# Optimization experiments

Measured on AMD Instinct MI355X. Metric: run time of the kernel, lower is better.

## Reference

```python
import jax, jax.numpy as jnp
import numpy as np

N = 50000   # nodes
E = 600000  # edges per relation
H = 4       # heads
DH = 32     # head dim (out_feat // num_heads)
D = 128     # in_feat == out_feat
NEG_SLOPE = 0.2


def setup_inputs() -> dict:
    key = jax.random.key(0)
    ks = jax.random.split(key, 13)
    x = jax.random.normal(ks[0], (N, D), jnp.float32)
    src_r0 = jax.random.randint(ks[1], (E,), 0, N, jnp.int32)
    dst_r0 = jax.random.randint(ks[2], (E,), 0, N, jnp.int32)
    src_r1 = jax.random.randint(ks[3], (E,), 0, N, jnp.int32)
    dst_r1 = jax.random.randint(ks[4], (E,), 0, N, jnp.int32)
    s = 0.05  # keep activations moderate (xavier-like scale)
    W_r0 = jax.random.normal(ks[5], (D, H * DH), jnp.float32) * s
    attn_l_r0 = jax.random.normal(ks[6], (H, DH), jnp.float32) * s
    attn_r_r0 = jax.random.normal(ks[7], (H, DH), jnp.float32) * s
    W_r1 = jax.random.normal(ks[8], (D, H * DH), jnp.float32) * s
    attn_l_r1 = jax.random.normal(ks[9], (H, DH), jnp.float32) * s
    attn_r_r1 = jax.random.normal(ks[10], (H, DH), jnp.float32) * s
    loop_weight = jax.random.normal(ks[11], (D, D), jnp.float32) * s
    h_bias = jnp.zeros((D,), jnp.float32)
    return {"x": x, "src_r0": src_r0, "dst_r0": dst_r0, "src_r1": src_r1,
            "dst_r1": dst_r1, "W_r0": W_r0, "attn_l_r0": attn_l_r0,
            "attn_r_r0": attn_r_r0, "W_r1": W_r1, "attn_l_r1": attn_l_r1,
            "attn_r_r1": attn_r_r1, "loop_weight": loop_weight, "h_bias": h_bias}


def _gat_rel(x, src, dst, W, attn_l, attn_r):
    """DGL GATConv for one relation: fc -> per-node attn scalars -> edge
    leaky_relu -> per-dst softmax -> weighted scatter-sum. Heads flattened."""
    feat = (x @ W).reshape(-1, H, DH)                 # [N, H, DH]
    el = jnp.einsum('nhd,hd->nh', feat, attn_l)       # [N, H]
    er = jnp.einsum('nhd,hd->nh', feat, attn_r)       # [N, H]
    e = jax.nn.leaky_relu(el[src] + er[dst], NEG_SLOPE)  # [E, H]
    # edge softmax per destination node, per head (numerically stable)
    m = jax.ops.segment_max(e, dst, num_segments=N)   # [N, H]
    ex = jnp.exp(e - m[dst])                          # [E, H]
    z = jax.ops.segment_sum(ex, dst, num_segments=N)  # [N, H]
    a = ex / z[dst]                                   # [E, H]
    msg = a[:, :, None] * feat[src]                   # [E, H, DH]
    out = jax.ops.segment_sum(msg, dst, num_segments=N)  # [N, H, DH]
    return out.reshape(-1, H * DH)                    # [N, D] (concat heads)


def reference(x, src_r0, dst_r0, src_r1, dst_r1, W_r0, attn_l_r0, attn_r_r0,
              W_r1, attn_l_r1, attn_r_r1, loop_weight, h_bias):
    # HeteroGraphConv with default 'sum' aggregation across relations
    h = _gat_rel(x, src_r0, dst_r0, W_r0, attn_l_r0, attn_r_r0)
    h = h + _gat_rel(x, src_r1, dst_r1, W_r1, attn_l_r1, attn_r_r1)
    # self-loop linear + bias + activation (dropout p=0.0 is identity)
    h = h + x @ loop_weight + h_bias
    return jax.nn.relu(h)
```

## Files before the change

### kernel.cpp

```cpp
#include <hip/hip_runtime.h>
#include <math.h>


#define CAP 48
#define NB 256
#define BCAP 2752
#define BIN_EDGES 2048

typedef __attribute__((ext_vector_type(8))) short short8v;
typedef __attribute__((ext_vector_type(4))) float float4v;

__device__ __forceinline__ unsigned short f2bf(float f) {
  unsigned int u = __float_as_uint(f);
  unsigned int r = (u + 0x7fffu + ((u >> 16) & 1u)) >> 16;
  return (unsigned short)r;
}
__device__ __forceinline__ float2 bfpair(unsigned int u) {
  float2 r;
  r.x = __uint_as_float(u << 16);
  r.y = __uint_as_float(u & 0xffff0000u);
  return r;
}

__global__ __launch_bounds__(256) void prep_bin_kernel(
    const float* __restrict__ W0, const float* __restrict__ W1,
    const float* __restrict__ WL,
    const float* __restrict__ al0, const float* __restrict__ ar0,
    const float* __restrict__ al1, const float* __restrict__ ar1,
    const int* __restrict__ src0, const int* __restrict__ dst0,
    const int* __restrict__ src1, const int* __restrict__ dst1,
    unsigned short* __restrict__ Wtall,
    unsigned int* __restrict__ bpair, int* __restrict__ gcnt,
    int E, int width, int nconvb, int nbin)
{
  __shared__ int smem[512];
  const int t = threadIdx.x;

  if ((int)blockIdx.x < nconvb) {
    const int j = blockIdx.x * 256 + t;
    if (j < 4096) {
      const int rel = j >> 11;
      const int q = j & 2047;
      const int n = q >> 4;
      const int k0 = (q & 15) * 8;
      const float* W = rel ? W1 : W0;
      unsigned short o[8];
#pragma unroll
      for (int u = 0; u < 8; ++u) o[u] = f2bf(W[(size_t)(k0 + u) * 128 + n]);
      *(short8v*)&Wtall[(size_t)rel * 18432 + n * 128 + k0] = *(short8v*)o;
    } else if (j < 4352) {
      const int e = j - 4096;
      const int rel = e >> 7;
      const int q = e & 127;
      const int cIdx = q >> 4;
      const int isr = cIdx >> 2;
      const int h = cIdx & 3;
      const int k0 = (q & 15) * 8;
      const float* W = rel ? W1 : W0;
      const float* av = isr ? (rel ? ar1 : ar0) : (rel ? al1 : al0);
      unsigned short o[8];
#pragma unroll
      for (int u = 0; u < 8; ++u) {
        float s = 0.f;
#pragma unroll
        for (int d = 0; d < 32; ++d)
          s += W[(size_t)(k0 + u) * 128 + h * 32 + d] * av[h * 32 + d];
        o[u] = f2bf(s);
      }
      *(short8v*)&Wtall[(size_t)rel * 18432 + (128 + cIdx) * 128 + k0] = *(short8v*)o;
    } else if (j < 4608) {
      const int e = j - 4352;
      const int rel = e >> 7;
      const int q = e & 127;
      const int cIdx = 136 + (q >> 4);
      const int k0 = (q & 15) * 8;
      const short8v z = {0,0,0,0,0,0,0,0};
      *(short8v*)&Wtall[(size_t)rel * 18432 + cIdx * 128 + k0] = z;
    } else if (j < 6656) {
      const int e = j - 4608;
      const int n = e >> 4;
      const int k0 = (e & 15) * 8;
      unsigned short o[8];
#pragma unroll
      for (int u = 0; u < 8; ++u) o[u] = f2bf(WL[(size_t)(k0 + u) * 128 + n]);
      *(short8v*)&Wtall[(size_t)2 * 18432 + n * 128 + k0] = *(short8v*)o;
    }
  } else {
    int* cnt = smem;
    int* gb  = smem + NB;
    const int bid = blockIdx.x - nconvb;
    const int rel = (bid >= nbin) ? 1 : 0;
    const int ib  = rel ? (bid - nbin) : bid;
    const int* srcA = rel ? src1 : src0;
    const int* dstA = rel ? dst1 : dst0;
    const int base = ib * BIN_EDGES;
    const int cntE = min(E - base, BIN_EDGES);

    for (int i = t; i < NB; i += 256) cnt[i] = 0;
    __syncthreads();

    unsigned int epack[8]; int eb[8], epos[8];
#pragma unroll
    for (int q = 0; q < 8; ++q) {
      const int ei = t * 8 + q;
      if (ei < cntE) {
        const int s = srcA[base + ei];
        const int d = dstA[base + ei];
        const int b = d / width;
        const int ld = d - b * width;
        epack[q] = (unsigned int)s | ((unsigned int)ld << 16);
        eb[q] = b;
        epos[q] = atomicAdd(&cnt[b], 1);
      } else {
        eb[q] = -1;
      }
    }
    __syncthreads();
    for (int i = t; i < NB; i += 256)
      gb[i] = atomicAdd(&gcnt[rel * NB + i], cnt[i]);
    __syncthreads();
#pragma unroll
    for (int q = 0; q < 8; ++q) {
      if (eb[q] >= 0) {
        const int slot = gb[eb[q]] + epos[q];
        if (slot < BCAP)
          bpair[(size_t)(rel * NB + eb[q]) * BCAP + slot] = epack[q];
      }
    }
  }
}

__global__ __launch_bounds__(256) void gemm_ell_kernel(
    const float* __restrict__ x, const unsigned short* __restrict__ Wtall,
    unsigned short* __restrict__ f0, unsigned short* __restrict__ f1,
    unsigned short* __restrict__ xl,
    float* __restrict__ el0, float* __restrict__ er0,
    float* __restrict__ el1, float* __restrict__ er1,
    const unsigned int* __restrict__ bpair, const int* __restrict__ gcnt,
    int* __restrict__ deg, int* __restrict__ ell0, int* __restrict__ ell1,
    int N, int width, int ngemm)
{
  __shared__ int ldeg[256];

  if ((int)blockIdx.x < ngemm) {
    const int wave = threadIdx.x >> 6, lane = threadIdx.x & 63;
    const int lr = lane & 15, lk = lane >> 4;
    const int row0 = blockIdx.x * 64 + wave * 16;
    const int r = row0 + lr;

    short8v a[4];
#pragma unroll
    for (int kc = 0; kc < 4; ++kc) {
      if (r < N) {
        const float* xp = &x[(size_t)r * 128 + kc * 32 + lk * 8];
        float4 u = *(const float4*)xp;
        float4 v = *(const float4*)(xp + 4);
        unsigned short o[8];
        o[0]=f2bf(u.x); o[1]=f2bf(u.y); o[2]=f2bf(u.z); o[3]=f2bf(u.w);
        o[4]=f2bf(v.x); o[5]=f2bf(v.y); o[6]=f2bf(v.z); o[7]=f2bf(v.w);
        a[kc] = *(short8v*)o;
      } else {
        a[kc] = (short8v){0,0,0,0,0,0,0,0};
      }
    }

#pragma unroll
    for (int w = 0; w < 3; ++w) {
      const unsigned short* Wp = Wtall + (size_t)w * 18432;
      const int NF = (w < 2) ? 9 : 8;
      float4v acc[9];
#pragma unroll
      for (int nf = 0; nf < 9; ++nf) acc[nf] = (float4v){0.f, 0.f, 0.f, 0.f};
      for (int nf = 0; nf < NF; ++nf) {
        const unsigned short* Bp = &Wp[(size_t)(nf * 16 + lr) * 128];
#pragma unroll
        for (int kc = 0; kc < 4; ++kc) {
          const short8v b = *(const short8v*)&Bp[kc * 32 + lk * 8];
          acc[nf] = __builtin_amdgcn_mfma_f32_16x16x32_bf16(a[kc], b, acc[nf], 0, 0, 0);
        }
      }

      unsigned short* dstp = (w == 0) ? f0 : (w == 1) ? f1 : xl;
#pragma unroll
      for (int nf = 0; nf < 8; ++nf) {
        const int col = nf * 16 + lr;
#pragma unroll
        for (int j = 0; j < 4; ++j) {
          const int row = row0 + lk * 4 + j;
          if (row < N) dstp[(size_t)row * 128 + col] = f2bf(acc[nf][j]);
        }
      }
      if (w < 2 && lr < 8) {
        float* ep = (lr < 4) ? (w ? el1 : el0) : (w ? er1 : er0);
        const int h = lr & 3;
#pragma unroll
        for (int j = 0; j < 4; ++j) {
          const int row = row0 + lk * 4 + j;
          if (row < N) ep[row * 4 + h] = acc[8][j];
        }
      }
    }
  } else {
    const int bid = blockIdx.x - ngemm;
    const int rel = bid >> 8;
    const int b = bid & 255;
    const int t = threadIdx.x;
    const int d0 = b * width;
    if (t < width) ldeg[t] = 0;
    __syncthreads();
    const int count = min(gcnt[rel * NB + b], BCAP);
    int* ell = rel ? ell1 : ell0;
    const unsigned int* bp = &bpair[(size_t)(rel * NB + b) * BCAP];
    for (int i = t; i < count; i += 256) {
      const unsigned int v = bp[i];
      const int src = (int)(v & 0xFFFFu);
      const int ld = (int)(v >> 16);
      const int slot = atomicAdd(&ldeg[ld], 1);
      if (slot < CAP) ell[(size_t)(d0 + ld) * CAP + slot] = src;
    }
    __syncthreads();
    if (t < width && d0 + t < N) deg[rel * N + d0 + t] = ldeg[t];
  }
}

__global__ __launch_bounds__(256) void gat_aggregate_kernel(
    const unsigned short* __restrict__ f0, const unsigned short* __restrict__ f1,
    const unsigned short* __restrict__ xl,
    const float* __restrict__ el0, const float* __restrict__ er0,
    const float* __restrict__ el1, const float* __restrict__ er1,
    const int* __restrict__ deg,
    const int* __restrict__ ell0, const int* __restrict__ ell1,
    const float* __restrict__ bias, float* __restrict__ out, int N)
{
  const int wid  = threadIdx.x >> 6;
  const int lane = threadIdx.x & 63;
  const int n = blockIdx.x * 4 + wid;
  if (n >= N) return;
  const int h  = lane >> 4;
  const int il = lane & 15;
  const int c  = lane * 2;
  const int pbase = lane & 48;

  float ox = 0.f, oy = 0.f;

#pragma unroll
  for (int rel = 0; rel < 2; ++rel) {
    const unsigned short* fb = rel ? f1 : f0;
    const float* el = rel ? el1 : el0;
    const float erh = (rel ? er1 : er0)[n * 4 + h];
    const int* ell = rel ? ell1 : ell0;
    const int d = min(deg[rel * N + n], CAP);

    float m = -INFINITY, sum = 0.f;
    float axa = 0.f, aya = 0.f, axb = 0.f, ayb = 0.f;
    for (int base = 0; base < d; base += 16) {
      const bool valid = (base + il) < d;
      int srcv = ell[(size_t)n * CAP + base + il];
      srcv = valid ? srcv : 0;
      float ev;
      {
        const float elv = el[srcv * 4 + h];
        float e2 = elv + erh;
        e2 = e2 > 0.f ? e2 : 0.2f * e2;
        ev = valid ? e2 : -INFINITY;
      }
      float cm = ev;
      cm = fmaxf(cm, __shfl_xor(cm, 1));
      cm = fmaxf(cm, __shfl_xor(cm, 2));
      cm = fmaxf(cm, __shfl_xor(cm, 4));
      cm = fmaxf(cm, __shfl_xor(cm, 8));
      const float mn = fmaxf(m, cm);
      const float scale = __expf(m - mn);
      const float p = __expf(ev - mn);
      float cs = p;
      cs += __shfl_xor(cs, 1);
      cs += __shfl_xor(cs, 2);
      cs += __shfl_xor(cs, 4);
      cs += __shfl_xor(cs, 8);
      sum = sum * scale + cs;
      m = mn;
      axa *= scale; aya *= scale; axb *= scale; ayb *= scale;

      unsigned int fu[16];
#pragma unroll
      for (int i = 0; i < 16; ++i) {
        const int s = __builtin_amdgcn_readlane(srcv, i);
        fu[i] = *(const unsigned int*)&fb[(size_t)s * 128 + c];
      }
#pragma unroll
      for (int i = 0; i < 16; i += 2) {
        const float pa = __shfl(p, pbase + i);
        const float pb = __shfl(p, pbase + i + 1);
        const float2 fva = bfpair(fu[i]);
        const float2 fvb = bfpair(fu[i + 1]);
        axa += pa * fva.x; aya += pa * fva.y;
        axb += pb * fvb.x; ayb += pb * fvb.y;
      }
    }
    if (d > 0) {
      const float inv = 1.f / sum;
      ox += (axa + axb) * inv;
      oy += (aya + ayb) * inv;
    }
  }

  const float2 xlv = bfpair(*(const unsigned int*)&xl[(size_t)n * 128 + c]);
  const float2 bv  = *(const float2*)&bias[c];
  ox += xlv.x + bv.x;
  oy += xlv.y + bv.y;
  float2 res;
  res.x = fmaxf(ox, 0.f);
  res.y = fmaxf(oy, 0.f);
  *(float2*)&out[(size_t)n * 128 + c] = res;
}

extern "C" void kernel_launch(void* const* d_in, const int* in_sizes, int n_in,
                              void* d_out, int out_size, void* d_ws, size_t ws_size,
                              hipStream_t stream)
{
  const int N = in_sizes[0] / 128;
  const int E = in_sizes[1];

  const float* x    = (const float*)d_in[0];
  const int* src0   = (const int*)d_in[1];
  const int* dst0   = (const int*)d_in[2];
  const int* src1   = (const int*)d_in[3];
  const int* dst1   = (const int*)d_in[4];
  const float* W0   = (const float*)d_in[5];
  const float* al0  = (const float*)d_in[6];
  const float* ar0  = (const float*)d_in[7];
  const float* W1   = (const float*)d_in[8];
  const float* al1  = (const float*)d_in[9];
  const float* ar1  = (const float*)d_in[10];
  const float* WL   = (const float*)d_in[11];
  const float* bias = (const float*)d_in[12];
  float* out = (float*)d_out;

  char* p = (char*)d_ws;
  auto alloc = [&](size_t bytes) { char* r = p; p += (bytes + 255) & ~(size_t)255; return r; };
  unsigned short* f0 = (unsigned short*)alloc((size_t)N * 128 * 2);
  unsigned short* f1 = (unsigned short*)alloc((size_t)N * 128 * 2);
  unsigned short* xl = (unsigned short*)alloc((size_t)N * 128 * 2);
  float* el0 = (float*)alloc((size_t)N * 4 * 4);
  float* er0 = (float*)alloc((size_t)N * 4 * 4);
  float* el1 = (float*)alloc((size_t)N * 4 * 4);
  float* er1 = (float*)alloc((size_t)N * 4 * 4);
  int* deg   = (int*)alloc((size_t)2 * N * 4);
  int* ell0  = (int*)alloc((size_t)CAP * N * 4);
  int* ell1  = (int*)alloc((size_t)CAP * N * 4);
  unsigned int* bpair = (unsigned int*)alloc((size_t)2 * NB * BCAP * 4);
  int* gcnt  = (int*)alloc((size_t)2 * NB * 4);
  unsigned short* Wtall = (unsigned short*)alloc((size_t)(2 * 144 + 128) * 128 * 2);

  const int width = (N + NB - 1) / NB;
  const int ngemm = (N + 63) / 64;
  const int nbin  = (E + BIN_EDGES - 1) / BIN_EDGES;
  const int nconvb = 26;

  hipMemsetAsync(gcnt, 0, (size_t)2 * NB * 4, stream);

  prep_bin_kernel<<<nconvb + 2 * nbin, 256, 0, stream>>>(
      W0, W1, WL, al0, ar0, al1, ar1, src0, dst0, src1, dst1,
      Wtall, bpair, gcnt, E, width, nconvb, nbin);

  gemm_ell_kernel<<<ngemm + 2 * NB, 256, 0, stream>>>(
      x, Wtall, f0, f1, xl, el0, er0, el1, er1,
      bpair, gcnt, deg, ell0, ell1, N, width, ngemm);

  gat_aggregate_kernel<<<(N + 3) / 4, 256, 0, stream>>>(
      f0, f1, xl, el0, er0, el1, er1, deg, ell0, ell1, bias, out, N);
}
```

Measured before the change: 159.6 us.

## Use 16-bit ELL indices, peel first aggregation chunk, and widen bin blocks

The ELL neighbour lists are stored as 16-bit indices instead of 32-bit, halving index traffic. The aggregate kernel now peels the first 16-neighbour chunk for both relations and issues all their feature gathers up front for more memory-level parallelism. It also broadcasts softmax weights through LDS instead of per-element shuffles. The binning kernel moves to 512-thread blocks covering 4096 edges each. 16-bit indices assume N fits in 65536, and the extra LDS round trips add some cost.

```diff
diff --git a/kernel.cpp b/kernel.cpp
--- a/kernel.cpp
+++ b/kernel.cpp
@@ -5,7 +5,7 @@
 #define CAP 48
 #define NB 256
 #define BCAP 2752
-#define BIN_EDGES 2048
+#define BIN_EDGES 4096
 
 typedef __attribute__((ext_vector_type(8))) short short8v;
 typedef __attribute__((ext_vector_type(4))) float float4v;
@@ -22,7 +22,7 @@
   return r;
 }
 
-__global__ __launch_bounds__(256) void prep_bin_kernel(
+__global__ __launch_bounds__(512) void prep_bin_kernel(
     const float* __restrict__ W0, const float* __restrict__ W1,
     const float* __restrict__ WL,
     const float* __restrict__ al0, const float* __restrict__ ar0,
@@ -37,7 +37,7 @@
   const int t = threadIdx.x;
 
   if ((int)blockIdx.x < nconvb) {
-    const int j = blockIdx.x * 256 + t;
+    const int j = blockIdx.x * 512 + t;
     if (j < 4096) {
       const int rel = j >> 11;
       const int q = j & 2047;
@@ -96,7 +96,7 @@
     const int base = ib * BIN_EDGES;
     const int cntE = min(E - base, BIN_EDGES);
 
-    for (int i = t; i < NB; i += 256) cnt[i] = 0;
+    for (int i = t; i < NB; i += 512) cnt[i] = 0;
     __syncthreads();
 
     unsigned int epack[8]; int eb[8], epos[8];
@@ -116,7 +116,7 @@
       }
     }
     __syncthreads();
-    for (int i = t; i < NB; i += 256)
+    for (int i = t; i < NB; i += 512)
       gb[i] = atomicAdd(&gcnt[rel * NB + i], cnt[i]);
     __syncthreads();
 #pragma unroll
@@ -137,7 +137,8 @@
     float* __restrict__ el0, float* __restrict__ er0,
     float* __restrict__ el1, float* __restrict__ er1,
     const unsigned int* __restrict__ bpair, const int* __restrict__ gcnt,
-    int* __restrict__ deg, int* __restrict__ ell0, int* __restrict__ ell1,
+    int* __restrict__ deg, unsigned short* __restrict__ ell0,
+    unsigned short* __restrict__ ell1,
     int N, int width, int ngemm)
 {
   __shared__ int ldeg[256];
@@ -209,14 +210,14 @@
     if (t < width) ldeg[t] = 0;
     __syncthreads();
     const int count = min(gcnt[rel * NB + b], BCAP);
-    int* ell = rel ? ell1 : ell0;
+    unsigned short* ell = rel ? ell1 : ell0;
     const unsigned int* bp = &bpair[(size_t)(rel * NB + b) * BCAP];
     for (int i = t; i < count; i += 256) {
       const unsigned int v = bp[i];
       const int src = (int)(v & 0xFFFFu);
       const int ld = (int)(v >> 16);
       const int slot = atomicAdd(&ldeg[ld], 1);
-      if (slot < CAP) ell[(size_t)(d0 + ld) * CAP + slot] = src;
+      if (slot < CAP) ell[(size_t)(d0 + ld) * CAP + slot] = (unsigned short)src;
     }
     __syncthreads();
     if (t < width && d0 + t < N) deg[rel * N + d0 + t] = ldeg[t];
@@ -229,9 +230,10 @@
     const float* __restrict__ el0, const float* __restrict__ er0,
     const float* __restrict__ el1, const float* __restrict__ er1,
     const int* __restrict__ deg,
-    const int* __restrict__ ell0, const int* __restrict__ ell1,
+    const unsigned short* __restrict__ ell0, const unsigned short* __restrict__ ell1,
     const float* __restrict__ bias, float* __restrict__ out, int N)
 {
+  __shared__ float p_lds[4][2][4][16];
   const int wid  = threadIdx.x >> 6;
   const int lane = threadIdx.x & 63;
   const int n = blockIdx.x * 4 + wid;
@@ -239,71 +241,144 @@
   const int h  = lane >> 4;
   const int il = lane & 15;
   const int c  = lane * 2;
-  const int pbase = lane & 48;
-
-  float ox = 0.f, oy = 0.f;
-
-#pragma unroll
-  for (int rel = 0; rel < 2; ++rel) {
-    const unsigned short* fb = rel ? f1 : f0;
-    const float* el = rel ? el1 : el0;
-    const float erh = (rel ? er1 : er0)[n * 4 + h];
-    const int* ell = rel ? ell1 : ell0;
-    const int d = min(deg[rel * N + n], CAP);
-
-    float m = -INFINITY, sum = 0.f;
-    float axa = 0.f, aya = 0.f, axb = 0.f, ayb = 0.f;
-    for (int base = 0; base < d; base += 16) {
+
+  const int rs0 = (int)ell0[(size_t)n * CAP + il];
+  const int rs1 = (int)ell1[(size_t)n * CAP + il];
+  const int d0 = min(deg[n], CAP);
+  const int d1 = min(deg[N + n], CAP);
+  const float er0h = er0[n * 4 + h];
+  const float er1h = er1[n * 4 + h];
+
+  const bool v0 = il < d0, v1 = il < d1;
+  const int s0 = v0 ? rs0 : 0;
+  const int s1 = v1 ? rs1 : 0;
+  const float elv0 = el0[s0 * 4 + h];
+  const float elv1 = el1[s1 * 4 + h];
+
+  float m0, sum0, m1, sum1;
+  {
+    float e = elv0 + er0h;  e = e > 0.f ? e : 0.2f * e;
+    float ev = v0 ? e : -INFINITY;
+    float cm = ev;
+    cm = fmaxf(cm, __shfl_xor(cm, 1)); cm = fmaxf(cm, __shfl_xor(cm, 2));
+    cm = fmaxf(cm, __shfl_xor(cm, 4)); cm = fmaxf(cm, __shfl_xor(cm, 8));
+    const float p = __expf(ev - cm);
+    float cs = p;
+    cs += __shfl_xor(cs, 1); cs += __shfl_xor(cs, 2);
+    cs += __shfl_xor(cs, 4); cs += __shfl_xor(cs, 8);
+    m0 = cm; sum0 = cs;
+    p_lds[wid][0][h][il] = p;
+  }
+  {
+    float e = elv1 + er1h;  e = e > 0.f ? e : 0.2f * e;
+    float ev = v1 ? e : -INFINITY;
+    float cm = ev;
+    cm = fmaxf(cm, __shfl_xor(cm, 1)); cm = fmaxf(cm, __shfl_xor(cm, 2));
+    cm = fmaxf(cm, __shfl_xor(cm, 4)); cm = fmaxf(cm, __shfl_xor(cm, 8));
+    const float p = __expf(ev - cm);
+    float cs = p;
+    cs += __shfl_xor(cs, 1); cs += __shfl_xor(cs, 2);
+    cs += __shfl_xor(cs, 4); cs += __shfl_xor(cs, 8);
+    m1 = cm; sum1 = cs;
+    p_lds[wid][1][h][il] = p;
+  }
+
+  unsigned int fu0[16], fu1[16];
+#pragma unroll
+  for (int i = 0; i < 16; ++i) {
+    const int s = __builtin_amdgcn_readlane(s0, i);
+    fu0[i] = *(const unsigned int*)&f0[(size_t)s * 128 + c];
+  }
+#pragma unroll
+  for (int i = 0; i < 16; ++i) {
+    const int s = __builtin_amdgcn_readlane(s1, i);
+    fu1[i] = *(const unsigned int*)&f1[(size_t)s * 128 + c];
+  }
+
+  float ax0 = 0.f, ay0 = 0.f;
+  {
+    float p16[16];
+    *(float4*)&p16[0]  = *(const float4*)&p_lds[wid][0][h][0];
+    *(float4*)&p16[4]  = *(const float4*)&p_lds[wid][0][h][4];
+    *(float4*)&p16[8]  = *(const float4*)&p_lds[wid][0][h][8];
+    *(float4*)&p16[12] = *(const float4*)&p_lds[wid][0][h][12];
+    float axa=0.f, aya=0.f, axb=0.f, ayb=0.f;
+#pragma unroll
+    for (int i = 0; i < 16; i += 2) {
+      const float2 fa = bfpair(fu0[i]);
+      const float2 fb2 = bfpair(fu0[i+1]);
+      axa += p16[i]*fa.x;   aya += p16[i]*fa.y;
+      axb += p16[i+1]*fb2.x; ayb += p16[i+1]*fb2.y;
+    }
+    ax0 = axa + axb; ay0 = aya + ayb;
+  }
+  float ax1 = 0.f, ay1 = 0.f;
+  {
+    float p16[16];
+    *(float4*)&p16[0]  = *(const float4*)&p_lds[wid][1][h][0];
+    *(float4*)&p16[4]  = *(const float4*)&p_lds[wid][1][h][4];
+    *(float4*)&p16[8]  = *(const float4*)&p_lds[wid][1][h][8];
+    *(float4*)&p16[12] = *(const float4*)&p_lds[wid][1][h][12];
+    float axa=0.f, aya=0.f, axb=0.f, ayb=0.f;
+#pragma unroll
+    for (int i = 0; i < 16; i += 2) {
+      const float2 fa = bfpair(fu1[i]);
+      const float2 fb2 = bfpair(fu1[i+1]);
+      axa += p16[i]*fa.x;   aya += p16[i]*fa.y;
+      axb += p16[i+1]*fb2.x; ayb += p16[i+1]*fb2.y;
+    }
+    ax1 = axa + axb; ay1 = aya + ayb;
+  }
+
+  auto tail = [&](const unsigned short* ellp, const float* elp, float erh,
+                  int d, const unsigned short* fbp, float& m, float& sum,
+                  float& ax, float& ay, int slot) {
+    for (int base = 16; base < d; base += 16) {
       const bool valid = (base + il) < d;
-      int srcv = ell[(size_t)n * CAP + base + il];
-      srcv = valid ? srcv : 0;
-      float ev;
-      {
-        const float elv = el[srcv * 4 + h];
-        float e2 = elv + erh;
-        e2 = e2 > 0.f ? e2 : 0.2f * e2;
-        ev = valid ? e2 : -INFINITY;
-      }
+      int sv = (int)ellp[(size_t)n * CAP + base + il];
+      sv = valid ? sv : 0;
+      const float elv = elp[sv * 4 + h];
+      float e = elv + erh; e = e > 0.f ? e : 0.2f * e;
+      const float ev = valid ? e : -INFINITY;
       float cm = ev;
-      cm = fmaxf(cm, __shfl_xor(cm, 1));
-      cm = fmaxf(cm, __shfl_xor(cm, 2));
-      cm = fmaxf(cm, __shfl_xor(cm, 4));
-      cm = fmaxf(cm, __shfl_xor(cm, 8));
+      cm = fmaxf(cm, __shfl_xor(cm, 1)); cm = fmaxf(cm, __shfl_xor(cm, 2));
+      cm = fmaxf(cm, __shfl_xor(cm, 4)); cm = fmaxf(cm, __shfl_xor(cm, 8));
       const float mn = fmaxf(m, cm);
       const float scale = __expf(m - mn);
       const float p = __expf(ev - mn);
       float cs = p;
-      cs += __shfl_xor(cs, 1);
-      cs += __shfl_xor(cs, 2);
-      cs += __shfl_xor(cs, 4);
-      cs += __shfl_xor(cs, 8);
+      cs += __shfl_xor(cs, 1); cs += __shfl_xor(cs, 2);
+      cs += __shfl_xor(cs, 4); cs += __shfl_xor(cs, 8);
       sum = sum * scale + cs;
       m = mn;
-      axa *= scale; aya *= scale; axb *= scale; ayb *= scale;
-
+      p_lds[wid][slot][h][il] = p;
       unsigned int fu[16];
 #pragma unroll
       for (int i = 0; i < 16; ++i) {
-        const int s = __builtin_amdgcn_readlane(srcv, i);
-        fu[i] = *(const unsigned int*)&fb[(size_t)s * 128 + c];
-      }
-#pragma unroll
-      for (int i = 0; i < 16; i += 2) {
-        const float pa = __shfl(p, pbase + i);
-        const float pb = __shfl(p, pbase + i + 1);
-        const float2 fva = bfpair(fu[i]);
-        const float2 fvb = bfpair(fu[i + 1]);
-        axa += pa * fva.x; aya += pa * fva.y;
-        axb += pb * fvb.x; ayb += pb * fvb.y;
-      }
-    }
-    if (d > 0) {
-      const float inv = 1.f / sum;
-      ox += (axa + axb) * inv;
-      oy += (aya + ayb) * inv;
-    }
-  }
-
+        const int s = __builtin_amdgcn_readlane(sv, i);
+        fu[i] = *(const unsigned int*)&fbp[(size_t)s * 128 + c];
+      }
+      float p16[16];
+      *(float4*)&p16[0]  = *(const float4*)&p_lds[wid][slot][h][0];
+      *(float4*)&p16[4]  = *(const float4*)&p_lds[wid][slot][h][4];
+      *(float4*)&p16[8]  = *(const float4*)&p_lds[wid][slot][h][8];
+      *(float4*)&p16[12] = *(const float4*)&p_lds[wid][slot][h][12];
+      float axa=0.f, aya=0.f;
+#pragma unroll
+      for (int i = 0; i < 16; ++i) {
+        const float2 f = bfpair(fu[i]);
+        axa += p16[i]*f.x; aya += p16[i]*f.y;
+      }
+      ax = ax * scale + axa;
+      ay = ay * scale + aya;
+    }
+  };
+  if (d0 > 16) tail(ell0, el0, er0h, d0, f0, m0, sum0, ax0, ay0, 0);
+  if (d1 > 16) tail(ell1, el1, er1h, d1, f1, m1, sum1, ax1, ay1, 1);
+
+  float ox = 0.f, oy = 0.f;
+  if (d0 > 0) { const float inv = 1.f / sum0; ox += ax0 * inv; oy += ay0 * inv; }
+  if (d1 > 0) { const float inv = 1.f / sum1; ox += ax1 * inv; oy += ay1 * inv; }
   const float2 xlv = bfpair(*(const unsigned int*)&xl[(size_t)n * 128 + c]);
   const float2 bv  = *(const float2*)&bias[c];
   ox += xlv.x + bv.x;
@@ -346,8 +421,8 @@
   float* el1 = (float*)alloc((size_t)N * 4 * 4);
   float* er1 = (float*)alloc((size_t)N * 4 * 4);
   int* deg   = (int*)alloc((size_t)2 * N * 4);
-  int* ell0  = (int*)alloc((size_t)CAP * N * 4);
-  int* ell1  = (int*)alloc((size_t)CAP * N * 4);
+  unsigned short* ell0 = (unsigned short*)alloc((size_t)CAP * N * 2);
+  unsigned short* ell1 = (unsigned short*)alloc((size_t)CAP * N * 2);
   unsigned int* bpair = (unsigned int*)alloc((size_t)2 * NB * BCAP * 4);
   int* gcnt  = (int*)alloc((size_t)2 * NB * 4);
   unsigned short* Wtall = (unsigned short*)alloc((size_t)(2 * 144 + 128) * 128 * 2);
@@ -355,11 +430,11 @@
   const int width = (N + NB - 1) / NB;
   const int ngemm = (N + 63) / 64;
   const int nbin  = (E + BIN_EDGES - 1) / BIN_EDGES;
-  const int nconvb = 26;
+  const int nconvb = 13;
 
   hipMemsetAsync(gcnt, 0, (size_t)2 * NB * 4, stream);
 
-  prep_bin_kernel<<<nconvb + 2 * nbin, 256, 0, stream>>>(
+  prep_bin_kernel<<<nconvb + 2 * nbin, 512, 0, stream>>>(
       W0, W1, WL, al0, ar0, al1, ar1, src0, dst0, src1, dst1,
       Wtall, bpair, gcnt, E, width, nconvb, nbin);
 
```

Result: faster. 153.4 us (-3.9%).
